# Optimization experiments

Measured on AMD Instinct MI355X. Metric: run time of the kernel, lower is better.

## Reference

```python
import jax, jax.numpy as jnp
import numpy as np

B, T, IN_DIM, H, W = 32, 20, 3, 1, 256
HID = 64
FC1_IN = HID * T * H * W  # 327680
FC1_OUT = 512
OUT_DIM = 3


def setup_inputs() -> dict:
    key = jax.random.key(0)
    ks = jax.random.split(key, 6)
    s = 0.02
    return dict(
        x=jax.random.normal(ks[0], (B, T, IN_DIM, H, W), dtype=jnp.float32),
        conv_w0=jax.random.normal(ks[1], (4 * HID, IN_DIM + HID, 3, 3), dtype=jnp.float32) * s,
        conv_b0=jnp.zeros((4 * HID,), dtype=jnp.float32),
        conv_w1=jax.random.normal(ks[2], (4 * HID, HID + HID, 3, 3), dtype=jnp.float32) * s,
        conv_b1=jnp.zeros((4 * HID,), dtype=jnp.float32),
        fc1_w=jax.random.normal(ks[3], (FC1_OUT, FC1_IN), dtype=jnp.float32) * s,
        fc1_b=jnp.zeros((FC1_OUT,), dtype=jnp.float32),
        fc2_w=jax.random.normal(ks[4], (OUT_DIM, FC1_OUT), dtype=jnp.float32) * s,
        fc2_b=jnp.zeros((OUT_DIM,), dtype=jnp.float32),
    )


def _convlstm_layer(inp, w, b):
    # inp: (B, T, C, H, W); w: (4*hid, C+hid, kh, kw)
    Bn, Tn, C, Hn, Wn = inp.shape
    hid = w.shape[0] // 4
    h0 = jnp.zeros((Bn, hid, Hn, Wn), inp.dtype)

    def step(carry, x_t):
        h, c = carry
        z = jnp.concatenate([x_t, h], axis=1)  # (B, C+hid, H, W)
        gates = jax.lax.conv_general_dilated(
            z, w, window_strides=(1, 1), padding='SAME',
            dimension_numbers=('NCHW', 'OIHW', 'NCHW')) + b[None, :, None, None]
        i, f, o, g = jnp.split(gates, 4, axis=1)
        c_new = jax.nn.sigmoid(f) * c + jax.nn.sigmoid(i) * jnp.tanh(g)
        h_new = jax.nn.sigmoid(o) * jnp.tanh(c_new)
        return (h_new, c_new), h_new

    _, hs = jax.lax.scan(step, (h0, h0), jnp.swapaxes(inp, 0, 1))
    return jnp.swapaxes(hs, 0, 1)  # (B, T, hid, H, W)


def reference(x, conv_w0, conv_b0, conv_w1, conv_b1, fc1_w, fc1_b, fc2_w, fc2_b):
    h = _convlstm_layer(x, conv_w0, conv_b0)
    h = _convlstm_layer(h, conv_w1, conv_b1)
    flat = h.reshape(h.shape[0], -1)  # (B, T*hid*H*W), torch .view order
    z = jax.nn.relu(flat @ fc1_w.T + fc1_b)
    out = z @ fc2_w.T + fc2_b
    return jnp.concatenate([out[:, :2], jax.nn.sigmoid(out[:, 2:])], axis=1)
```

## Files before the change

### kernel.cpp

```cpp
#include <hip/hip_runtime.h>
#include <hip/hip_bf16.h>
#include <cstddef>

#define BATCH 32
#define TSTEPS 20
#define IN_DIM 3
#define WIDTH 256
#define HID 64
#define FC1_IN 327680
#define FC1_OUT 512
#define OUT_DIM 3

#define CST 5
#define MARG 6
#define REGC 44
#define CORE 6
#define ROWS 50
#define CROWS 48

typedef _Float16 half8 __attribute__((ext_vector_type(8)));
typedef float floatx4 __attribute__((ext_vector_type(4)));

__device__ __forceinline__ float sigm(float x) {
    return 1.0f / (1.0f + __expf(-x));
}
__device__ __forceinline__ float tanh_fast(float x) {
    return 1.0f - 2.0f / (__expf(2.0f * x) + 1.0f);
}


__global__ __launch_bounds__(256) void prep_w0(
    const float* __restrict__ cw0, _Float16* __restrict__ wt0)
{
    int e = blockIdx.x * 256 + threadIdx.x;
    if (e >= 256 * 96) return;
    int co = e / 96, cip = e - co * 96;
    int ci = (cip < 64) ? (3 + cip) : (cip < 67 ? cip - 64 : -1);
    float v[3] = {0.f, 0.f, 0.f};
    if (ci >= 0) {
#pragma unroll
        for (int kw = 0; kw < 3; ++kw)
            v[kw] = cw0[(size_t)(co * 67 + ci) * 9 + 3 + kw];
    }
#pragma unroll
    for (int kw = 0; kw < 3; ++kw)
        wt0[(size_t)(kw * 256 + co) * 96 + cip] = (_Float16)v[kw];
}

__global__ __launch_bounds__(256) void prep_w1(
    const float* __restrict__ cw1, _Float16* __restrict__ wt1)
{
    int e = blockIdx.x * 256 + threadIdx.x;
    int co = e >> 7, ci = e & 127;
#pragma unroll
    for (int kw = 0; kw < 3; ++kw)
        wt1[(size_t)(kw * 256 + co) * 128 + ci] =
            (_Float16)cw1[(size_t)(co * 128 + ci) * 9 + 3 + kw];
}

__global__ __launch_bounds__(256) void prep_x(
    const float* __restrict__ x, _Float16* __restrict__ xT)
{
    int e = blockIdx.x * 256 + threadIdx.x;
    if (e >= TSTEPS * BATCH * WIDTH) return;
    int t = e / (BATCH * WIDTH);
    int rem = e - t * BATCH * WIDTH;
    int b = rem >> 8, w = rem & 255;
    half8 v = {};
#pragma unroll
    for (int ci = 0; ci < 3; ++ci)
        v[ci] = (_Float16)x[(size_t)((b * TSTEPS + t) * IN_DIM + ci) * WIDTH + w];
    *(half8*)&xT[(size_t)e * 8] = v;
}

__global__ __launch_bounds__(512) void conv_chunk(
    const _Float16* __restrict__ xT,
    const _Float16* __restrict__ wt0,
    const _Float16* __restrict__ wt1,
    const float* __restrict__ cb0,
    const float* __restrict__ cb1,
    _Float16* __restrict__ fcin,
    _Float16* __restrict__ h0g,
    _Float16* __restrict__ h1g,
    float* __restrict__ c0g,
    float* __restrict__ c1g,
    int t0, int first, int save)
{
    __shared__ __align__(16) _Float16 h0s[2][ROWS * 64];
    __shared__ __align__(16) _Float16 h1s[2][ROWS * 64];
    __shared__ __align__(16) _Float16 xs[2][ROWS * 8];
    __shared__ float c0s[CROWS * 64];
    __shared__ float c1s[CROWS * 64];
    __shared__ __align__(16) _Float16 zero16[8];

    const int b    = blockIdx.x;
    const int w0   = blockIdx.y * 32;
    const int tid  = threadIdx.x;
    const int wave = tid >> 6;
    const int ln = tid & 63;
    const int lr = ln & 15;
    const int kg = ln >> 4;

    {
        _Float16* h0f = &h0s[0][0];
        _Float16* h1f = &h1s[0][0];
        for (int i = tid; i < 2 * ROWS * 64; i += 512) { h0f[i] = (_Float16)0.0f; h1f[i] = (_Float16)0.0f; }
        for (int i = tid; i < CROWS * 64; i += 512) { c0s[i] = 0.0f; c1s[i] = 0.0f; }
        for (int i = tid; i < ROWS * 8; i += 512) xs[1][i] = (_Float16)0.0f;
        if (tid < 8) zero16[tid] = (_Float16)0.0f;
    }
    __syncthreads();

    {
        if (tid < ROWS) {
            int w = w0 - 7 + tid;
            half8 v = {};
            if (w >= 0 && w < WIDTH)
                v = *(const half8*)&xT[((size_t)(t0 * BATCH + b) * WIDTH + w) * 8];
            *(half8*)&xs[0][tid * 8] = v;
        }
        if (!first) {
            for (int i = tid; i < REGC * 8; i += 512) {
                int row = 1 + (i >> 3), c = i & 7;
                int w = w0 - 7 + row;
                half8 v0 = {}, v1 = {};
                if (w >= 0 && w < WIDTH) {
                    v0 = *(const half8*)&h0g[((size_t)b * WIDTH + w) * 64 + c * 8];
                    v1 = *(const half8*)&h1g[((size_t)b * WIDTH + w) * 64 + c * 8];
                }
                int phys = c ^ (row & 7);
                *(half8*)&h0s[1][row * 64 + phys * 8] = v0;
                *(half8*)&h1s[1][row * 64 + phys * 8] = v1;
            }
            for (int i = tid; i < REGC * 64; i += 512) {
                int n = i >> 6, hc = i & 63;
                int w = w0 - 6 + n;
                float v0 = 0.f, v1 = 0.f;
                if (w >= 0 && w < WIDTH) {
                    v0 = c0g[((size_t)b * WIDTH + w) * 64 + hc];
                    v1 = c1g[((size_t)b * WIDTH + w) * 64 + hc];
                }
                int ci = n * 64 + (hc ^ (((n >> 2) & 3) << 4));
                c0s[ci] = v0;
                c1s[ci] = v1;
            }
        }
    }

    if (wave < 4) {
        const int hc = wave * 16 + lr;

        half8 b0r[3][3][4];
#pragma unroll
        for (int kw = 0; kw < 3; ++kw)
#pragma unroll
        for (int kf = 0; kf < 3; ++kf)
#pragma unroll
        for (int cf = 0; cf < 4; ++cf)
            b0r[kw][kf][cf] = *(const half8*)&wt0[
                (size_t)(kw * 256 + cf * 64 + hc) * 96 + kf * 32 + kg * 8];

        float cbr0[4];
#pragma unroll
        for (int cf = 0; cf < 4; ++cf) cbr0[cf] = cb0[cf * 64 + hc];

        __syncthreads();

        for (int p = 0; p <= CST; ++p) {
            const int rd = (p ^ 1) & 1;
            const int wr = p & 1;
            half8 xreg = {};
            const bool xst = (p < CST - 1) && (tid < ROWS);
            if (xst) {
                int w = w0 - 7 + tid;
                if (w >= 0 && w < WIDTH)
                    xreg = *(const half8*)&xT[((size_t)((t0 + p + 1) * BATCH + b) * WIDTH + w) * 8];
            }
            if (p < CST) {
#pragma unroll
                for (int j = 0; j < 3; ++j) {
                    floatx4 acc[4];
#pragma unroll
                    for (int cf = 0; cf < 4; ++cf) acc[cf] = (floatx4)0.0f;
#pragma unroll
                    for (int kw = 0; kw < 3; ++kw)
#pragma unroll
                    for (int kf = 0; kf < 3; ++kf) {
                        int row = 16 * j + lr + kw;
                        half8 a;
                        if (kf < 2) {
                            int phys = (kf * 4 + kg) ^ (row & 7);
                            a = *(const half8*)&h0s[rd][row * 64 + phys * 8];
                        } else {
                            a = (kg == 0) ? *(const half8*)&xs[wr][row * 8]
                                          : *(const half8*)&zero16[0];
                        }
#pragma unroll
                        for (int cf = 0; cf < 4; ++cf)
                            acc[cf] = __builtin_amdgcn_mfma_f32_16x16x32_f16(a, b0r[kw][kf][cf], acc[cf], 0, 0, 0);
                    }
#pragma unroll
                    for (int r = 0; r < 4; ++r) {
                        int n = 16 * j + kg * 4 + r;
                        int cidx = n * 64 + (hc ^ (kg << 4));
                        float cv = c0s[cidx];
                        float cn = sigm(acc[1][r] + cbr0[1]) * cv
                                 + sigm(acc[0][r] + cbr0[0]) * tanh_fast(acc[3][r] + cbr0[3]);
                        c0s[cidx] = cn;
                        int w = w0 - 6 + n;
                        if (w >= 0 && w < WIDTH) {
                            _Float16 hv = (_Float16)(sigm(acc[2][r] + cbr0[2]) * tanh_fast(cn));
                            int rowo = n + 1;
                            int phys = (hc >> 3) ^ (rowo & 7);
                            *((_Float16*)((char*)&h0s[wr][0] + rowo * 128 + phys * 16 + (hc & 7) * 2)) = hv;
                        }
                    }
                }
            }
            if (xst) *(half8*)&xs[(p + 1) & 1][tid * 8] = xreg;
            __syncthreads();
        }
    } else {
        const int hc = (wave - 4) * 16 + lr;

        half8 b1r[3][4][4];
#pragma unroll
        for (int kw = 0; kw < 3; ++kw)
#pragma unroll
        for (int kf = 0; kf < 4; ++kf)
#pragma unroll
        for (int cf = 0; cf < 4; ++cf)
            b1r[kw][kf][cf] = *(const half8*)&wt1[
                (size_t)(kw * 256 + cf * 64 + hc) * 128 + kf * 32 + kg * 8];

        float cbr1[4];
#pragma unroll
        for (int cf = 0; cf < 4; ++cf) cbr1[cf] = cb1[cf * 64 + hc];

        __syncthreads();

        for (int p = 0; p <= CST; ++p) {
            const int rd   = (p ^ 1) & 1;
            const int h1rd = p & 1;
            if (p >= 1) {
#pragma unroll
                for (int j = 0; j < 3; ++j) {
                    floatx4 acc[4];
#pragma unroll
                    for (int cf = 0; cf < 4; ++cf) acc[cf] = (floatx4)0.0f;
#pragma unroll
                    for (int kw = 0; kw < 3; ++kw)
#pragma unroll
                    for (int kf = 0; kf < 4; ++kf) {
                        int row = 16 * j + lr + kw;
                        half8 a;
                        if (kf < 2) {
                            int phys = (kf * 4 + kg) ^ (row & 7);
                            a = *(const half8*)&h0s[rd][row * 64 + phys * 8];
                        } else {
                            int phys = ((kf - 2) * 4 + kg) ^ (row & 7);
                            a = *(const half8*)&h1s[h1rd][row * 64 + phys * 8];
                        }
#pragma unroll
                        for (int cf = 0; cf < 4; ++cf)
                            acc[cf] = __builtin_amdgcn_mfma_f32_16x16x32_f16(a, b1r[kw][kf][cf], acc[cf], 0, 0, 0);
                    }
#pragma unroll
                    for (int r = 0; r < 4; ++r) {
                        int n = 16 * j + kg * 4 + r;
                        int cidx = n * 64 + (hc ^ (kg << 4));
                        float cv = c1s[cidx];
                        float cn = sigm(acc[1][r] + cbr1[1]) * cv
                                 + sigm(acc[0][r] + cbr1[0]) * tanh_fast(acc[3][r] + cbr1[3]);
                        c1s[cidx] = cn;
                        _Float16 hv = (_Float16)(sigm(acc[2][r] + cbr1[2]) * tanh_fast(cn));
                        int w = w0 - 6 + n;
                        if (w >= 0 && w < WIDTH) {
                            int rowo = n + 1;
                            int phys = (hc >> 3) ^ (rowo & 7);
                            *((_Float16*)((char*)&h1s[rd][0] + rowo * 128 + phys * 16 + (hc & 7) * 2)) = hv;
                        }
                        if (n >= CORE && n < CORE + 32)
                            fcin[(size_t)b * FC1_IN + (size_t)((t0 + p - 1) * HID + hc) * WIDTH + w] = hv;
                    }
                }
            }
            __syncthreads();
        }
    }

    if (save) {
        for (int i = tid; i < 32 * 64; i += 512) {
            int n = CORE + (i >> 6);
            int hc = i & 63;
            int w = w0 + (i >> 6);
            int rowo = n + 1;
            int physh = (hc >> 3) ^ (rowo & 7);
            h0g[((size_t)b * WIDTH + w) * 64 + hc] = h0s[0][rowo * 64 + physh * 8 + (hc & 7)];
            h1g[((size_t)b * WIDTH + w) * 64 + hc] = h1s[0][rowo * 64 + physh * 8 + (hc & 7)];
            int ci = n * 64 + (hc ^ (((n >> 2) & 3) << 4));
            c0g[((size_t)b * WIDTH + w) * 64 + hc] = c0s[ci];
            c1g[((size_t)b * WIDTH + w) * 64 + hc] = c1s[ci];
        }
    }
}

#define KSLICE 1280
#define KPHASE 640
#define NSPLIT 256
#define ALDS_STRIDE 648

__global__ __launch_bounds__(512) void fc1_mfma(
    const _Float16* __restrict__ a,
    const float* __restrict__ w,
    float* __restrict__ part)
{
    __shared__ _Float16 alds[32][ALDS_STRIDE];

    const int blk = blockIdx.x;
    const int tid = threadIdx.x;
    const int wv  = tid >> 6;
    const int ln  = tid & 63;
    const int lg  = ln >> 4;
    const int lr  = ln & 15;
    const int k0  = blk * KSLICE;

    floatx4 acc[2][4];
#pragma unroll
    for (int bt = 0; bt < 2; ++bt)
#pragma unroll
        for (int nt = 0; nt < 4; ++nt) acc[bt][nt] = (floatx4)0.0f;

    const float* wbase[4];
#pragma unroll
    for (int nt = 0; nt < 4; ++nt)
        wbase[nt] = w + (size_t)(wv * 64 + nt * 16 + lr) * FC1_IN + k0 + lg * 8;

    for (int p = 0; p < 2; ++p) {
        __syncthreads();
        for (int i = tid; i < 32 * 80; i += 512) {
            int r = i / 80;
            int c = (i - r * 80) * 8;
            *(half8*)&alds[r][c] =
                *(const half8*)&a[(size_t)r * FC1_IN + k0 + p * KPHASE + c];
        }
        __syncthreads();

        for (int kc = 0; kc < KPHASE / 32; ++kc) {
            half8 af0 = *(const half8*)&alds[lr][kc * 32 + lg * 8];
            half8 af1 = *(const half8*)&alds[16 + lr][kc * 32 + lg * 8];
#pragma unroll
            for (int nt = 0; nt < 4; ++nt) {
                const float* wp = wbase[nt] + p * KPHASE + kc * 32;
                float4 wlo = *(const float4*)wp;
                float4 whi = *(const float4*)(wp + 4);
                half8 bf;
                bf[0] = (_Float16)wlo.x; bf[1] = (_Float16)wlo.y;
                bf[2] = (_Float16)wlo.z; bf[3] = (_Float16)wlo.w;
                bf[4] = (_Float16)whi.x; bf[5] = (_Float16)whi.y;
                bf[6] = (_Float16)whi.z; bf[7] = (_Float16)whi.w;
                acc[0][nt] = __builtin_amdgcn_mfma_f32_16x16x32_f16(af0, bf, acc[0][nt], 0, 0, 0);
                acc[1][nt] = __builtin_amdgcn_mfma_f32_16x16x32_f16(af1, bf, acc[1][nt], 0, 0, 0);
            }
        }
    }

#pragma unroll
    for (int bt = 0; bt < 2; ++bt)
#pragma unroll
        for (int nt = 0; nt < 4; ++nt) {
            int n = wv * 64 + nt * 16 + lr;
            int b = bt * 16 + lg * 4;
            *(float4*)&part[((size_t)blk * FC1_OUT + n) * BATCH + b] =
                *(float4*)&acc[bt][nt];
        }
}

__global__ __launch_bounds__(256) void fc1_reduce(
    const float* __restrict__ part, const float* __restrict__ b1,
    float* __restrict__ z1)
{
    int e = blockIdx.x * 256 + threadIdx.x;
    float s = 0.0f;
    for (int ks = 0; ks < NSPLIT; ++ks)
        s += part[(size_t)ks * (FC1_OUT * BATCH) + e];
    int n = e >> 5, b = e & 31;
    float v = s + b1[n];
    z1[(size_t)b * FC1_OUT + n] = v > 0.0f ? v : 0.0f;
}

__global__ __launch_bounds__(128) void fc2_kernel(
    const float* __restrict__ z1, const float* __restrict__ w2,
    const float* __restrict__ b2, float* __restrict__ out)
{
    int t = threadIdx.x;
    if (t >= BATCH * OUT_DIM) return;
    int b = t / OUT_DIM, n = t - b * OUT_DIM;
    const float* zr = z1 + (size_t)b * FC1_OUT;
    const float* wr = w2 + (size_t)n * FC1_OUT;
    float acc = b2[n];
    for (int k = 0; k < FC1_OUT; ++k) acc += zr[k] * wr[k];
    if (n == 2) acc = sigm(acc);
    out[(size_t)b * OUT_DIM + n] = acc;
}

extern "C" void kernel_launch(void* const* d_in, const int* in_sizes, int n_in,
                              void* d_out, int out_size, void* d_ws, size_t ws_size,
                              hipStream_t stream) {
    const float* x   = (const float*)d_in[0];
    const float* cw0 = (const float*)d_in[1];
    const float* cb0 = (const float*)d_in[2];
    const float* cw1 = (const float*)d_in[3];
    const float* cb1 = (const float*)d_in[4];
    const float* w1  = (const float*)d_in[5];
    const float* b1  = (const float*)d_in[6];
    const float* w2  = (const float*)d_in[7];
    const float* b2  = (const float*)d_in[8];
    float* out = (float*)d_out;

    const size_t S = (size_t)BATCH * WIDTH * HID;
    char* p = (char*)d_ws;
    auto alloc = [&](size_t bytes) { char* r = p; p += (bytes + 255) & ~(size_t)255; return r; };

    _Float16* wt0  = (_Float16*)alloc((size_t)3 * 256 * 96 * 2);
    _Float16* wt1  = (_Float16*)alloc((size_t)3 * 256 * 128 * 2);
    _Float16* xT   = (_Float16*)alloc((size_t)TSTEPS * BATCH * WIDTH * 8 * 2);
    _Float16* fcin = (_Float16*)alloc((size_t)BATCH * FC1_IN * 2);
    _Float16* h0g  = (_Float16*)alloc(S * 2);
    _Float16* h1g  = (_Float16*)alloc(S * 2);
    float*    c0g  = (float*)alloc(S * 4);
    float*    c1g  = (float*)alloc(S * 4);
    float*    part = (float*)alloc((size_t)NSPLIT * FC1_OUT * BATCH * 4);
    float*    z1   = (float*)alloc((size_t)BATCH * FC1_OUT * 4);

    prep_w0<<<96, 256, 0, stream>>>(cw0, wt0);
    prep_w1<<<128, 256, 0, stream>>>(cw1, wt1);
    prep_x<<<(TSTEPS * BATCH * WIDTH + 255) / 256, 256, 0, stream>>>(x, xT);

    for (int k = 0; k < 4; ++k) {
        conv_chunk<<<dim3(BATCH, 8), 512, 0, stream>>>(
            xT, wt0, wt1, cb0, cb1, fcin, h0g, h1g, c0g, c1g,
            k * CST, (k == 0) ? 1 : 0, (k < 3) ? 1 : 0);
    }

    fc1_mfma<<<NSPLIT, 512, 0, stream>>>(fcin, w1, part);
    fc1_reduce<<<64, 256, 0, stream>>>(part, b1, z1);
    fc2_kernel<<<1, 128, 0, stream>>>(z1, w2, b2, out);
}
```

Before: 435.1 us.

## Overlap fc1 K-slices with later ConvLSTM chunks in a combined launch

Merges the fc1 split-K GEMM into the conv chunk kernel. Each launch after the first adds 128 extra blocks that compute fc1 partial sums for the timesteps finished by the previous chunk, while the conv blocks advance the recurrence. A tail launch handles the last chunk. The memory-bound fc1 weight streaming can then run on CU capacity the latency-bound recurrence leaves idle. The split is doubled to 512 slices of 640, so the reduction reads twice as many partials, and conv and fc1 blocks now compete for CU and memory resources. s_setprio is also raised around the conv MFMA loops so that work keeps priority.

```diff
diff --git a/kernel.cpp b/kernel.cpp
--- a/kernel.cpp
+++ b/kernel.cpp
@@ -18,6 +18,9 @@
 #define ROWS 50
 #define CROWS 48
 
+#define KSLICE 640
+#define NSPLIT 512
+
 typedef _Float16 half8 __attribute__((ext_vector_type(8)));
 typedef float floatx4 __attribute__((ext_vector_type(4)));
 
@@ -73,7 +76,7 @@
     *(half8*)&xT[(size_t)e * 8] = v;
 }
 
-__global__ __launch_bounds__(512) void conv_chunk(
+__global__ __launch_bounds__(512) void conv_fc1(
     const _Float16* __restrict__ xT,
     const _Float16* __restrict__ wt0,
     const _Float16* __restrict__ wt1,
@@ -84,30 +87,90 @@
     _Float16* __restrict__ h1g,
     float* __restrict__ c0g,
     float* __restrict__ c1g,
-    int t0, int first, int save)
-{
-    __shared__ __align__(16) _Float16 h0s[2][ROWS * 64];
-    __shared__ __align__(16) _Float16 h1s[2][ROWS * 64];
-    __shared__ __align__(16) _Float16 xs[2][ROWS * 8];
-    __shared__ float c0s[CROWS * 64];
-    __shared__ float c1s[CROWS * 64];
-    __shared__ __align__(16) _Float16 zero16[8];
-
-    const int b    = blockIdx.x;
-    const int w0   = blockIdx.y * 32;
-    const int tid  = threadIdx.x;
-    const int wave = tid >> 6;
+    const float* __restrict__ w1,
+    float* __restrict__ part,
+    int t0, int first, int save, int ks_base)
+{
+    __shared__ __align__(16) char smem[51840];
+
+    const int bid = blockIdx.x;
+    const int tid = threadIdx.x;
     const int ln = tid & 63;
     const int lr = ln & 15;
     const int kg = ln >> 4;
 
+    if (bid >= 256) {
+        _Float16* alds = (_Float16*)smem;
+        const int ks = ks_base + (bid - 256);
+        const int wv = tid >> 6;
+        const int lg = kg;
+        const int k0 = ks * KSLICE;
+
+        floatx4 acc[2][4];
+#pragma unroll
+        for (int bt = 0; bt < 2; ++bt)
+#pragma unroll
+            for (int nt = 0; nt < 4; ++nt) acc[bt][nt] = (floatx4)0.0f;
+
+        const float* wbase[4];
+#pragma unroll
+        for (int nt = 0; nt < 4; ++nt)
+            wbase[nt] = w1 + (size_t)(wv * 64 + nt * 16 + lr) * FC1_IN + k0 + lg * 8;
+
+        for (int i = tid; i < 32 * 80; i += 512) {
+            int r = i / 80;
+            int c = (i - r * 80) * 8;
+            *(half8*)&alds[r * 648 + c] =
+                *(const half8*)&fcin[(size_t)r * FC1_IN + k0 + c];
+        }
+        __syncthreads();
+
+        for (int kc = 0; kc < KSLICE / 32; ++kc) {
+            half8 af0 = *(const half8*)&alds[lr * 648 + kc * 32 + lg * 8];
+            half8 af1 = *(const half8*)&alds[(16 + lr) * 648 + kc * 32 + lg * 8];
+#pragma unroll
+            for (int nt = 0; nt < 4; ++nt) {
+                const float* wp = wbase[nt] + kc * 32;
+                float4 wlo = *(const float4*)wp;
+                float4 whi = *(const float4*)(wp + 4);
+                half8 bf;
+                bf[0] = (_Float16)wlo.x; bf[1] = (_Float16)wlo.y;
+                bf[2] = (_Float16)wlo.z; bf[3] = (_Float16)wlo.w;
+                bf[4] = (_Float16)whi.x; bf[5] = (_Float16)whi.y;
+                bf[6] = (_Float16)whi.z; bf[7] = (_Float16)whi.w;
+                acc[0][nt] = __builtin_amdgcn_mfma_f32_16x16x32_f16(af0, bf, acc[0][nt], 0, 0, 0);
+                acc[1][nt] = __builtin_amdgcn_mfma_f32_16x16x32_f16(af1, bf, acc[1][nt], 0, 0, 0);
+            }
+        }
+
+#pragma unroll
+        for (int bt = 0; bt < 2; ++bt)
+#pragma unroll
+            for (int nt = 0; nt < 4; ++nt) {
+                int n = wv * 64 + nt * 16 + lr;
+                int bb = bt * 16 + lg * 4;
+                *(float4*)&part[((size_t)ks * FC1_OUT + n) * BATCH + bb] =
+                    *(float4*)&acc[bt][nt];
+            }
+        return;
+    }
+
+    _Float16* h0s = (_Float16*)smem;
+    _Float16* h1s = (_Float16*)(smem + 12800);
+    _Float16* xsp = (_Float16*)(smem + 25600);
+    float*    c0s = (float*)(smem + 27200);
+    float*    c1s = (float*)(smem + 39488);
+    _Float16* z16 = (_Float16*)(smem + 51776);
+
+    const int b    = bid & 31;
+    const int w0   = (bid >> 5) * 32;
+    const int wave = tid >> 6;
+
     {
-        _Float16* h0f = &h0s[0][0];
-        _Float16* h1f = &h1s[0][0];
-        for (int i = tid; i < 2 * ROWS * 64; i += 512) { h0f[i] = (_Float16)0.0f; h1f[i] = (_Float16)0.0f; }
+        for (int i = tid; i < 2 * ROWS * 64; i += 512) { h0s[i] = (_Float16)0.0f; h1s[i] = (_Float16)0.0f; }
         for (int i = tid; i < CROWS * 64; i += 512) { c0s[i] = 0.0f; c1s[i] = 0.0f; }
-        for (int i = tid; i < ROWS * 8; i += 512) xs[1][i] = (_Float16)0.0f;
-        if (tid < 8) zero16[tid] = (_Float16)0.0f;
+        for (int i = tid; i < ROWS * 8; i += 512) xsp[400 + i] = (_Float16)0.0f;
+        if (tid < 8) z16[tid] = (_Float16)0.0f;
     }
     __syncthreads();
 
@@ -117,7 +180,7 @@
             half8 v = {};
             if (w >= 0 && w < WIDTH)
                 v = *(const half8*)&xT[((size_t)(t0 * BATCH + b) * WIDTH + w) * 8];
-            *(half8*)&xs[0][tid * 8] = v;
+            *(half8*)&xsp[tid * 8] = v;
         }
         if (!first) {
             for (int i = tid; i < REGC * 8; i += 512) {
@@ -129,8 +192,8 @@
                     v1 = *(const half8*)&h1g[((size_t)b * WIDTH + w) * 64 + c * 8];
                 }
                 int phys = c ^ (row & 7);
-                *(half8*)&h0s[1][row * 64 + phys * 8] = v0;
-                *(half8*)&h1s[1][row * 64 + phys * 8] = v1;
+                *(half8*)&h0s[3200 + row * 64 + phys * 8] = v0;
+                *(half8*)&h1s[3200 + row * 64 + phys * 8] = v1;
             }
             for (int i = tid; i < REGC * 64; i += 512) {
                 int n = i >> 6, hc = i & 63;
@@ -182,6 +245,7 @@
                     floatx4 acc[4];
 #pragma unroll
                     for (int cf = 0; cf < 4; ++cf) acc[cf] = (floatx4)0.0f;
+                    __builtin_amdgcn_s_setprio(1);
 #pragma unroll
                     for (int kw = 0; kw < 3; ++kw)
 #pragma unroll
@@ -190,15 +254,16 @@
                         half8 a;
                         if (kf < 2) {
                             int phys = (kf * 4 + kg) ^ (row & 7);
-                            a = *(const half8*)&h0s[rd][row * 64 + phys * 8];
+                            a = *(const half8*)&h0s[rd * 3200 + row * 64 + phys * 8];
                         } else {
-                            a = (kg == 0) ? *(const half8*)&xs[wr][row * 8]
-                                          : *(const half8*)&zero16[0];
+                            a = (kg == 0) ? *(const half8*)&xsp[wr * 400 + row * 8]
+                                          : *(const half8*)&z16[0];
                         }
 #pragma unroll
                         for (int cf = 0; cf < 4; ++cf)
                             acc[cf] = __builtin_amdgcn_mfma_f32_16x16x32_f16(a, b0r[kw][kf][cf], acc[cf], 0, 0, 0);
                     }
+                    __builtin_amdgcn_s_setprio(0);
 #pragma unroll
                     for (int r = 0; r < 4; ++r) {
                         int n = 16 * j + kg * 4 + r;
@@ -212,12 +277,12 @@
                             _Float16 hv = (_Float16)(sigm(acc[2][r] + cbr0[2]) * tanh_fast(cn));
                             int rowo = n + 1;
                             int phys = (hc >> 3) ^ (rowo & 7);
-                            *((_Float16*)((char*)&h0s[wr][0] + rowo * 128 + phys * 16 + (hc & 7) * 2)) = hv;
+                            *((_Float16*)((char*)(h0s + wr * 3200) + rowo * 128 + phys * 16 + (hc & 7) * 2)) = hv;
                         }
                     }
                 }
             }
-            if (xst) *(half8*)&xs[(p + 1) & 1][tid * 8] = xreg;
+            if (xst) *(half8*)&xsp[((p + 1) & 1) * 400 + tid * 8] = xreg;
             __syncthreads();
         }
     } else {
@@ -248,6 +313,7 @@
                     floatx4 acc[4];
 #pragma unroll
                     for (int cf = 0; cf < 4; ++cf) acc[cf] = (floatx4)0.0f;
+                    __builtin_amdgcn_s_setprio(1);
 #pragma unroll
                     for (int kw = 0; kw < 3; ++kw)
 #pragma unroll
@@ -256,15 +322,16 @@
                         half8 a;
                         if (kf < 2) {
                             int phys = (kf * 4 + kg) ^ (row & 7);
-                            a = *(const half8*)&h0s[rd][row * 64 + phys * 8];
+                            a = *(const half8*)&h0s[rd * 3200 + row * 64 + phys * 8];
                         } else {
                             int phys = ((kf - 2) * 4 + kg) ^ (row & 7);
-                            a = *(const half8*)&h1s[h1rd][row * 64 + phys * 8];
+                            a = *(const half8*)&h1s[h1rd * 3200 + row * 64 + phys * 8];
                         }
 #pragma unroll
                         for (int cf = 0; cf < 4; ++cf)
                             acc[cf] = __builtin_amdgcn_mfma_f32_16x16x32_f16(a, b1r[kw][kf][cf], acc[cf], 0, 0, 0);
                     }
+                    __builtin_amdgcn_s_setprio(0);
 #pragma unroll
                     for (int r = 0; r < 4; ++r) {
                         int n = 16 * j + kg * 4 + r;
@@ -278,7 +345,7 @@
                         if (w >= 0 && w < WIDTH) {
                             int rowo = n + 1;
                             int phys = (hc >> 3) ^ (rowo & 7);
-                            *((_Float16*)((char*)&h1s[rd][0] + rowo * 128 + phys * 16 + (hc & 7) * 2)) = hv;
+                            *((_Float16*)((char*)(h1s + rd * 3200) + rowo * 128 + phys * 16 + (hc & 7) * 2)) = hv;
                         }
                         if (n >= CORE && n < CORE + 32)
                             fcin[(size_t)b * FC1_IN + (size_t)((t0 + p - 1) * HID + hc) * WIDTH + w] = hv;
@@ -296,8 +363,8 @@
             int w = w0 + (i >> 6);
             int rowo = n + 1;
             int physh = (hc >> 3) ^ (rowo & 7);
-            h0g[((size_t)b * WIDTH + w) * 64 + hc] = h0s[0][rowo * 64 + physh * 8 + (hc & 7)];
-            h1g[((size_t)b * WIDTH + w) * 64 + hc] = h1s[0][rowo * 64 + physh * 8 + (hc & 7)];
+            h0g[((size_t)b * WIDTH + w) * 64 + hc] = h0s[rowo * 64 + physh * 8 + (hc & 7)];
+            h1g[((size_t)b * WIDTH + w) * 64 + hc] = h1s[rowo * 64 + physh * 8 + (hc & 7)];
             int ci = n * 64 + (hc ^ (((n >> 2) & 3) << 4));
             c0g[((size_t)b * WIDTH + w) * 64 + hc] = c0s[ci];
             c1g[((size_t)b * WIDTH + w) * 64 + hc] = c1s[ci];
@@ -305,25 +372,19 @@
     }
 }
 
-#define KSLICE 1280
-#define KPHASE 640
-#define NSPLIT 256
-#define ALDS_STRIDE 648
-
-__global__ __launch_bounds__(512) void fc1_mfma(
-    const _Float16* __restrict__ a,
-    const float* __restrict__ w,
-    float* __restrict__ part)
-{
-    __shared__ _Float16 alds[32][ALDS_STRIDE];
-
-    const int blk = blockIdx.x;
+__global__ __launch_bounds__(512) void fc1_tail(
+    const _Float16* __restrict__ a, const float* __restrict__ w,
+    float* __restrict__ part, int ks_base)
+{
+    __shared__ _Float16 alds[32 * 648];
+
+    const int ks = ks_base + blockIdx.x;
     const int tid = threadIdx.x;
-    const int wv  = tid >> 6;
-    const int ln  = tid & 63;
-    const int lg  = ln >> 4;
-    const int lr  = ln & 15;
-    const int k0  = blk * KSLICE;
+    const int wv = tid >> 6;
+    const int ln = tid & 63;
+    const int lg = ln >> 4;
+    const int lr = ln & 15;
+    const int k0 = ks * KSLICE;
 
     floatx4 acc[2][4];
 #pragma unroll
@@ -336,32 +397,28 @@
     for (int nt = 0; nt < 4; ++nt)
         wbase[nt] = w + (size_t)(wv * 64 + nt * 16 + lr) * FC1_IN + k0 + lg * 8;
 
-    for (int p = 0; p < 2; ++p) {
-        __syncthreads();
-        for (int i = tid; i < 32 * 80; i += 512) {
-            int r = i / 80;
-            int c = (i - r * 80) * 8;
-            *(half8*)&alds[r][c] =
-                *(const half8*)&a[(size_t)r * FC1_IN + k0 + p * KPHASE + c];
-        }
-        __syncthreads();
-
-        for (int kc = 0; kc < KPHASE / 32; ++kc) {
-            half8 af0 = *(const half8*)&alds[lr][kc * 32 + lg * 8];
-            half8 af1 = *(const half8*)&alds[16 + lr][kc * 32 + lg * 8];
-#pragma unroll
-            for (int nt = 0; nt < 4; ++nt) {
-                const float* wp = wbase[nt] + p * KPHASE + kc * 32;
-                float4 wlo = *(const float4*)wp;
-                float4 whi = *(const float4*)(wp + 4);
-                half8 bf;
-                bf[0] = (_Float16)wlo.x; bf[1] = (_Float16)wlo.y;
-                bf[2] = (_Float16)wlo.z; bf[3] = (_Float16)wlo.w;
-                bf[4] = (_Float16)whi.x; bf[5] = (_Float16)whi.y;
-                bf[6] = (_Float16)whi.z; bf[7] = (_Float16)whi.w;
-                acc[0][nt] = __builtin_amdgcn_mfma_f32_16x16x32_f16(af0, bf, acc[0][nt], 0, 0, 0);
-                acc[1][nt] = __builtin_amdgcn_mfma_f32_16x16x32_f16(af1, bf, acc[1][nt], 0, 0, 0);
-            }
+    for (int i = tid; i < 32 * 80; i += 512) {
+        int r = i / 80;
+        int c = (i - r * 80) * 8;
+        *(half8*)&alds[r * 648 + c] = *(const half8*)&a[(size_t)r * FC1_IN + k0 + c];
+    }
+    __syncthreads();
+
+    for (int kc = 0; kc < KSLICE / 32; ++kc) {
+        half8 af0 = *(const half8*)&alds[lr * 648 + kc * 32 + lg * 8];
+        half8 af1 = *(const half8*)&alds[(16 + lr) * 648 + kc * 32 + lg * 8];
+#pragma unroll
+        for (int nt = 0; nt < 4; ++nt) {
+            const float* wp = wbase[nt] + kc * 32;
+            float4 wlo = *(const float4*)wp;
+            float4 whi = *(const float4*)(wp + 4);
+            half8 bf;
+            bf[0] = (_Float16)wlo.x; bf[1] = (_Float16)wlo.y;
+            bf[2] = (_Float16)wlo.z; bf[3] = (_Float16)wlo.w;
+            bf[4] = (_Float16)whi.x; bf[5] = (_Float16)whi.y;
+            bf[6] = (_Float16)whi.z; bf[7] = (_Float16)whi.w;
+            acc[0][nt] = __builtin_amdgcn_mfma_f32_16x16x32_f16(af0, bf, acc[0][nt], 0, 0, 0);
+            acc[1][nt] = __builtin_amdgcn_mfma_f32_16x16x32_f16(af1, bf, acc[1][nt], 0, 0, 0);
         }
     }
 
@@ -371,7 +428,7 @@
         for (int nt = 0; nt < 4; ++nt) {
             int n = wv * 64 + nt * 16 + lr;
             int b = bt * 16 + lg * 4;
-            *(float4*)&part[((size_t)blk * FC1_OUT + n) * BATCH + b] =
+            *(float4*)&part[((size_t)ks * FC1_OUT + n) * BATCH + b] =
                 *(float4*)&acc[bt][nt];
         }
 }
@@ -438,12 +495,14 @@
     prep_x<<<(TSTEPS * BATCH * WIDTH + 255) / 256, 256, 0, stream>>>(x, xT);
 
     for (int k = 0; k < 4; ++k) {
-        conv_chunk<<<dim3(BATCH, 8), 512, 0, stream>>>(
+        int grid = (k == 0) ? 256 : 384;
+        conv_fc1<<<grid, 512, 0, stream>>>(
             xT, wt0, wt1, cb0, cb1, fcin, h0g, h1g, c0g, c1g,
-            k * CST, (k == 0) ? 1 : 0, (k < 3) ? 1 : 0);
-    }
-
-    fc1_mfma<<<NSPLIT, 512, 0, stream>>>(fcin, w1, part);
+            w1, part,
+            k * CST, (k == 0) ? 1 : 0, (k < 3) ? 1 : 0, (k - 1) * 128);
+    }
+    fc1_tail<<<128, 512, 0, stream>>>(fcin, w1, part, 384);
+
     fc1_reduce<<<64, 256, 0, stream>>>(part, b1, z1);
     fc2_kernel<<<1, 128, 0, stream>>>(z1, w2, b2, out);
 }
```

Measured after the change: 505.2 us. 1.16x slower.
